# Performance work log

Hardware: AMD Instinct MI355X
Metric: run time of the kernel (lower is better)

The kernel has to match this reference:

```python
import jax, jax.numpy as jnp
import numpy as np

DIM = 1024
HEADS = 16
HEAD_DIM = DIM // HEADS


def setup_inputs() -> dict:
    key = jax.random.key(0)
    ks = jax.random.split(key, 9)
    s = 1.0 / np.sqrt(DIM)
    return {
        "x": jax.random.normal(ks[0], (2, 2048, DIM), dtype=jnp.float32),
        "Wq": jax.random.normal(ks[1], (DIM, DIM), dtype=jnp.float32) * s,
        "bq": jnp.zeros((DIM,), dtype=jnp.float32),
        "Wk": jax.random.normal(ks[2], (DIM, DIM), dtype=jnp.float32) * s,
        "bk": jnp.zeros((DIM,), dtype=jnp.float32),
        "Wv": jax.random.normal(ks[3], (DIM, DIM), dtype=jnp.float32) * s,
        "bv": jnp.zeros((DIM,), dtype=jnp.float32),
        "Wo": jax.random.normal(ks[4], (DIM, DIM), dtype=jnp.float32) * s,
        "bo": jnp.zeros((DIM,), dtype=jnp.float32),
    }


def reference(x, Wq, bq, Wk, bk, Wv, bv, Wo, bo):
    B, S, D = x.shape
    H, Dh = HEADS, HEAD_DIM

    def split_heads(t):  # (B,S,D) -> (B,H,S,Dh)
        return t.reshape(B, S, H, Dh).transpose(0, 2, 1, 3)

    q = split_heads(x @ Wq + bq)
    k = split_heads(x @ Wk + bk)
    v = split_heads(x @ Wv + bv)

    scores = jnp.einsum("bhsd,bhtd->bhst", q, k) / np.sqrt(Dh).astype(x.dtype)
    attn = jax.nn.softmax(scores, axis=-1)
    ctx = jnp.einsum("bhst,bhtd->bhsd", attn, v)
    ctx = ctx.transpose(0, 2, 1, 3).reshape(B, S, D)
    return ctx @ Wo + bo
```

## Files before the change

### kernel.cpp

```cpp
#include <hip/hip_runtime.h>
#include <hip/hip_bf16.h>
#include <cstdint>

typedef __bf16 bf16;
typedef __bf16 bf16x8 __attribute__((ext_vector_type(8)));
typedef float f32x4 __attribute__((ext_vector_type(4)));
typedef float f32x8 __attribute__((ext_vector_type(8)));
typedef float f32x16 __attribute__((ext_vector_type(16)));

#define DIM   1024
#define SEQ   2048
#define BATCH 2
#define HEADS 16
#define HDIM  64

#define QSCALE 0.1803368801111204f

__device__ __forceinline__ void gload_lds16(const void* g, void* l) {
    __builtin_amdgcn_global_load_lds(
        (const __attribute__((address_space(1))) void*)g,
        (__attribute__((address_space(3))) void*)l,
        16, 0, 0);
}

__device__ __forceinline__ uint32_t pkbf(float a, float b) {
    union { bf16 h[2]; uint32_t u; } t;
    t.h[0] = (bf16)a; t.h[1] = (bf16)b;
    return t.u;
}

#define LO8(v)  __builtin_shufflevector(v, v, 0, 1, 2, 3, 4, 5, 6, 7)
#define HI8(v)  __builtin_shufflevector(v, v, 8, 9, 10, 11, 12, 13, 14, 15)
#define LO4(v)  __builtin_shufflevector(v, v, 0, 1, 2, 3)
#define HI4(v)  __builtin_shufflevector(v, v, 4, 5, 6, 7)

__global__ __launch_bounds__(256) void cvt_x_kernel(const float* __restrict__ x,
                                                    bf16* __restrict__ xb) {
    int idx = blockIdx.x * 256 + threadIdx.x;
    const float4* p = (const float4*)(x + (size_t)idx * 8);
    float4 a = p[0], b = p[1];
    bf16x8 o;
    o[0] = (bf16)a.x; o[1] = (bf16)a.y; o[2] = (bf16)a.z; o[3] = (bf16)a.w;
    o[4] = (bf16)b.x; o[5] = (bf16)b.y; o[6] = (bf16)b.z; o[7] = (bf16)b.w;
    *(bf16x8*)(xb + (size_t)idx * 8) = o;
}

__global__ __launch_bounds__(256) void cvt_wt_kernel(const float* __restrict__ Wq,
                                                     const float* __restrict__ Wk,
                                                     const float* __restrict__ Wv,
                                                     const float* __restrict__ Wo,
                                                     bf16* __restrict__ Wt) {
    int z = blockIdx.z;
    const float* W = (z == 0) ? Wq : (z == 1) ? Wk : (z == 2) ? Wv : Wo;
    bf16* out = Wt + (size_t)z * DIM * DIM;
    int w = threadIdx.x >> 6, lane = threadIdx.x & 63;
    int n  = blockIdx.x * 64 + lane;
    int kb = blockIdx.y * 32 + w * 8;
    bf16x8 o;
#pragma unroll
    for (int j = 0; j < 8; ++j)
        o[j] = (bf16)W[(size_t)(kb + j) * DIM + n];
    *(bf16x8*)(out + (size_t)n * DIM + kb) = o;
}

template <int MODE>
__global__ __launch_bounds__(256) void gemm128_kernel(
        const bf16* __restrict__ A,
        const bf16* __restrict__ WtB,
        const float* __restrict__ b0,
        const float* __restrict__ b1,
        const float* __restrict__ b2,
        void* __restrict__ outp) {
    constexpr int K = DIM;
    int z = (MODE == 0) ? blockIdx.z : 0;
    const bf16* Bt = WtB + (size_t)z * DIM * DIM;
    const float* bias = (MODE == 0) ? ((z == 0) ? b0 : (z == 1) ? b1 : b2) : b0;

    int m0 = blockIdx.y * 128, n0 = blockIdx.x * 128;
    int tid = threadIdx.x;
    int w = tid >> 6, lane = tid & 63, l15 = lane & 15, l4 = lane >> 4;
    int wr = (w >> 1) * 64, wc = (w & 1) * 64;

    __shared__ __align__(16) bf16 As[128 * 32];
    __shared__ __align__(16) bf16 Bs[128 * 32];

    f32x4 acc[4][4] = {};

    for (int k0 = 0; k0 < K; k0 += 32) {
#pragma unroll
        for (int r = 0; r < 2; ++r) {
            int c = r * 256 + tid;
            gload_lds16(A  + (size_t)(m0 + (c >> 2)) * K + k0 + (c & 3) * 8, &As[c * 8]);
            gload_lds16(Bt + (size_t)(n0 + (c >> 2)) * K + k0 + (c & 3) * 8, &Bs[c * 8]);
        }
        __syncthreads();
        bf16x8 af[4], bfr[4];
#pragma unroll
        for (int m = 0; m < 4; ++m)
            af[m] = *(const bf16x8*)&As[(wr + m * 16 + l15) * 32 + l4 * 8];
#pragma unroll
        for (int n = 0; n < 4; ++n)
            bfr[n] = *(const bf16x8*)&Bs[(wc + n * 16 + l15) * 32 + l4 * 8];
#pragma unroll
        for (int m = 0; m < 4; ++m)
#pragma unroll
            for (int n = 0; n < 4; ++n)
                acc[m][n] = __builtin_amdgcn_mfma_f32_16x16x32_bf16(
                    af[m], bfr[n], acc[m][n], 0, 0, 0);
        __syncthreads();
    }

    float oscale = (MODE == 0 && z == 0) ? QSCALE : 1.0f;
#pragma unroll
    for (int n = 0; n < 4; ++n) {
        int col = n0 + wc + n * 16 + l15;
        float bv = bias[col];
#pragma unroll
        for (int m = 0; m < 4; ++m) {
            int rowb = m0 + wr + m * 16 + l4 * 4;
            if (MODE == 1) {
                float* out = (float*)outp;
#pragma unroll
                for (int i = 0; i < 4; ++i)
                    out[(size_t)(rowb + i) * DIM + col] = acc[m][n][i] + bv;
            } else if (z < 2) {
                bf16* out = (bf16*)outp + (size_t)z * (BATCH * HEADS * SEQ * HDIM);
                int h = col >> 6, d = col & 63;
#pragma unroll
                for (int i = 0; i < 4; ++i) {
                    int row = rowb + i;
                    int bb = row >> 11, s = row & 2047;
                    out[(((size_t)(bb * HEADS + h)) * SEQ + s) * HDIM + d] =
                        (bf16)((acc[m][n][i] + bv) * oscale);
                }
            } else {
                bf16* out = (bf16*)outp + (size_t)2 * (BATCH * HEADS * SEQ * HDIM);
                int h = col >> 6, d = col & 63;
                int bb = rowb >> 11, s0 = rowb & 2047;
                union { bf16 hh[4]; ushort4 v; } pk;
#pragma unroll
                for (int i = 0; i < 4; ++i) pk.hh[i] = (bf16)(acc[m][n][i] + bv);
                *(ushort4*)&out[(((size_t)(bb * HEADS + h)) * HDIM + d) * SEQ + s0] = pk.v;
            }
        }
    }
}

__global__ __launch_bounds__(256) void attn_kernel(const bf16* __restrict__ Q,
                                                   const bf16* __restrict__ K,
                                                   const bf16* __restrict__ Vt,
                                                   bf16* __restrict__ ctx) {
    int hb = blockIdx.y;
    int bb = hb >> 4, h = hb & 15;
    int q0 = blockIdx.x * 128;
    int tid = threadIdx.x, w = tid >> 6, lane = tid & 63;
    int l31 = lane & 31, hi = lane >> 5;

    const bf16* Qh = Q  + (size_t)hb * SEQ * HDIM;
    const bf16* Kh = K  + (size_t)hb * SEQ * HDIM;
    const bf16* Vh = Vt + (size_t)hb * HDIM * SEQ;

    __shared__ __align__(16) bf16 Ks[2][64 * 64];
    __shared__ __align__(16) bf16 Vs[2][64 * 64];

    int qrow = q0 + w * 32 + l31;
    bf16x8 qf[4];
#pragma unroll
    for (int ks = 0; ks < 4; ++ks)
        qf[ks] = *(const bf16x8*)&Qh[(size_t)qrow * HDIM + ks * 16 + hi * 8];

    f32x16 o0 = {}, o1 = {};
    float l = 0.f;

    const bf16* kbase[2];
    const bf16* vbase[2];
    int ldsoff[2];
#pragma unroll
    for (int r = 0; r < 2; ++r) {
        int c = r * 256 + tid, row = c >> 3, sj = (c & 7) ^ (row & 7);
        kbase[r] = Kh + (size_t)row * HDIM + sj * 8;
        vbase[r] = Vh + (size_t)row * SEQ + sj * 8;
        ldsoff[r] = c * 8;
    }
    auto stage = [&](bf16* ksd, bf16* vsd, int kv0) {
#pragma unroll
        for (int r = 0; r < 2; ++r) {
            gload_lds16(kbase[r] + kv0 * HDIM, ksd + ldsoff[r]);
            gload_lds16(vbase[r] + kv0,        vsd + ldsoff[r]);
        }
    };

    int koffA = l31 * 128;
    int cb[4];
#pragma unroll
    for (int ks = 0; ks < 4; ++ks)
        cb[ks] = ((2 * ks + hi) ^ (l31 & 7)) << 4;

    auto proc = [&](const char* ksb, const char* vsb) {
        f32x16 s0 = {}, s1 = {};
        __builtin_amdgcn_s_setprio(1);
#pragma unroll
        for (int ks = 0; ks < 4; ++ks) {
            bf16x8 k0 = *(const bf16x8*)(ksb + koffA + cb[ks]);
            bf16x8 k1 = *(const bf16x8*)(ksb + koffA + 4096 + cb[ks]);
            s0 = __builtin_amdgcn_mfma_f32_32x32x16_bf16(k0, qf[ks], s0, 0, 0, 0);
            s1 = __builtin_amdgcn_mfma_f32_32x32x16_bf16(k1, qf[ks], s1, 0, 0, 0);
        }
        __builtin_amdgcn_s_setprio(0);

#pragma unroll
        for (int r = 0; r < 16; ++r) {
            s0[r] = __builtin_amdgcn_exp2f(s0[r]);
            s1[r] = __builtin_amdgcn_exp2f(s1[r]);
        }

        f32x16 a16 = s0 + s1;
        f32x8  a8  = LO8(a16) + HI8(a16);
        f32x4  a4  = LO4(a8) + HI4(a8);
        l += (a4[0] + a4[1]) + (a4[2] + a4[3]);

        bf16x8 pa[4];
#pragma unroll
        for (int f = 0; f < 4; ++f) {
            const f32x16& s = (f < 2) ? s0 : s1;
            int rb = (f & 1) * 8;
            uint32_t w0 = pkbf(s[rb + 0], s[rb + 1]), w1 = pkbf(s[rb + 2], s[rb + 3]);
            uint32_t w2 = pkbf(s[rb + 4], s[rb + 5]), w3 = pkbf(s[rb + 6], s[rb + 7]);
            asm("v_permlane32_swap_b32 %0, %1" : "+v"(w0), "+v"(w2));
            asm("v_permlane32_swap_b32 %0, %1" : "+v"(w1), "+v"(w3));
            union { uint32_t u[4]; bf16x8 v; } t2;
            t2.u[0] = w0; t2.u[1] = w1; t2.u[2] = w2; t2.u[3] = w3;
            pa[f] = t2.v;
        }

        __builtin_amdgcn_s_setprio(1);
#pragma unroll
        for (int ks = 0; ks < 4; ++ks) {
            bf16x8 v0 = *(const bf16x8*)(vsb + koffA + cb[ks]);
            bf16x8 v1 = *(const bf16x8*)(vsb + koffA + 4096 + cb[ks]);
            o0 = __builtin_amdgcn_mfma_f32_32x32x16_bf16(v0, pa[ks], o0, 0, 0, 0);
            o1 = __builtin_amdgcn_mfma_f32_32x32x16_bf16(v1, pa[ks], o1, 0, 0, 0);
        }
        __builtin_amdgcn_s_setprio(0);
    };

    constexpr int NT = SEQ / 64;
    stage(Ks[0], Vs[0], 0);
    __syncthreads();

    for (int t = 0; t < NT; t += 2) {
        if (t + 1 < NT) stage(Ks[1], Vs[1], (t + 1) * 64);
        proc((const char*)&Ks[0][0], (const char*)&Vs[0][0]);
        __syncthreads();
        if (t + 2 < NT) stage(Ks[0], Vs[0], (t + 2) * 64);
        proc((const char*)&Ks[1][0], (const char*)&Vs[1][0]);
        __syncthreads();
    }

    l += __shfl_xor(l, 32);
    float inv = 1.0f / l;
    size_t base = ((size_t)bb * SEQ + q0 + w * 32 + l31) * DIM + h * HDIM;
#pragma unroll
    for (int g = 0; g < 4; ++g) {
        int dh0 = 8 * g + 4 * hi;
        union { bf16 hh[4]; ushort4 u; } a, b2;
#pragma unroll
        for (int i = 0; i < 4; ++i) {
            a.hh[i]  = (bf16)(o0[4 * g + i] * inv);
            b2.hh[i] = (bf16)(o1[4 * g + i] * inv);
        }
        *(ushort4*)&ctx[base + dh0]      = a.u;
        *(ushort4*)&ctx[base + 32 + dh0] = b2.u;
    }
}

extern "C" void kernel_launch(void* const* d_in, const int* in_sizes, int n_in,
                              void* d_out, int out_size, void* d_ws, size_t ws_size,
                              hipStream_t stream) {
    const float* x  = (const float*)d_in[0];
    const float* Wq = (const float*)d_in[1];
    const float* bq = (const float*)d_in[2];
    const float* Wk = (const float*)d_in[3];
    const float* bk = (const float*)d_in[4];
    const float* Wv = (const float*)d_in[5];
    const float* bv = (const float*)d_in[6];
    const float* Wo = (const float*)d_in[7];
    const float* bo = (const float*)d_in[8];

    char* ws = (char*)d_ws;
    bf16* xb  = (bf16*)(ws);
    bf16* Wt  = (bf16*)(ws + (8u  << 20));
    bf16* Qb  = (bf16*)(ws + (16u << 20));
    bf16* Kb  = (bf16*)(ws + (24u << 20));
    bf16* Vb  = (bf16*)(ws + (32u << 20));
    bf16* ctx = (bf16*)(ws + (40u << 20));

    cvt_x_kernel<<<2048, 256, 0, stream>>>(x, xb);
    cvt_wt_kernel<<<dim3(16, 32, 4), 256, 0, stream>>>(Wq, Wk, Wv, Wo, Wt);
    gemm128_kernel<0><<<dim3(8, 32, 3), 256, 0, stream>>>(xb, Wt, bq, bk, bv, (void*)Qb);
    attn_kernel<<<dim3(16, 32), 256, 0, stream>>>(Qb, Kb, Vb, ctx);
    gemm128_kernel<1><<<dim3(8, 32, 1), 256, 0, stream>>>(
        ctx, Wt + (size_t)3 * DIM * DIM, bo, bo, bo, (void*)d_out);
}
```

Baseline: 125.2 us.

## Load K/V fragments directly from global into registers, dropping LDS staging

```diff
diff --git a/kernel.cpp b/kernel.cpp
--- a/kernel.cpp
+++ b/kernel.cpp
@@ -146,10 +146,12 @@
     }
 }
 
-__global__ __launch_bounds__(256) void attn_kernel(const bf16* __restrict__ Q,
-                                                   const bf16* __restrict__ K,
-                                                   const bf16* __restrict__ Vt,
-                                                   bf16* __restrict__ ctx) {
+struct KVFrags { bf16x8 k0[4], k1[4], v0[4], v1[4]; };
+
+__global__ __launch_bounds__(256, 2) void attn_kernel(const bf16* __restrict__ Q,
+                                                      const bf16* __restrict__ K,
+                                                      const bf16* __restrict__ Vt,
+                                                      bf16* __restrict__ ctx) {
     int hb = blockIdx.y;
     int bb = hb >> 4, h = hb & 15;
     int q0 = blockIdx.x * 128;
@@ -157,11 +159,8 @@
     int l31 = lane & 31, hi = lane >> 5;
 
     const bf16* Qh = Q  + (size_t)hb * SEQ * HDIM;
-    const bf16* Kh = K  + (size_t)hb * SEQ * HDIM;
-    const bf16* Vh = Vt + (size_t)hb * HDIM * SEQ;
-
-    __shared__ __align__(16) bf16 Ks[2][64 * 64];
-    __shared__ __align__(16) bf16 Vs[2][64 * 64];
+    const bf16* kbase = K  + (size_t)hb * SEQ * HDIM + (size_t)l31 * HDIM + hi * 8;
+    const bf16* vbase = Vt + (size_t)hb * HDIM * SEQ + (size_t)l31 * SEQ  + hi * 8;
 
     int qrow = q0 + w * 32 + l31;
     bf16x8 qf[4];
@@ -172,39 +171,25 @@
     f32x16 o0 = {}, o1 = {};
     float l = 0.f;
 
-    const bf16* kbase[2];
-    const bf16* vbase[2];
-    int ldsoff[2];
-#pragma unroll
-    for (int r = 0; r < 2; ++r) {
-        int c = r * 256 + tid, row = c >> 3, sj = (c & 7) ^ (row & 7);
-        kbase[r] = Kh + (size_t)row * HDIM + sj * 8;
-        vbase[r] = Vh + (size_t)row * SEQ + sj * 8;
-        ldsoff[r] = c * 8;
-    }
-    auto stage = [&](bf16* ksd, bf16* vsd, int kv0) {
-#pragma unroll
-        for (int r = 0; r < 2; ++r) {
-            gload_lds16(kbase[r] + kv0 * HDIM, ksd + ldsoff[r]);
-            gload_lds16(vbase[r] + kv0,        vsd + ldsoff[r]);
+    auto load = [&](KVFrags& f, int kv0) {
+        const bf16* kp = kbase + (size_t)kv0 * HDIM;
+        const bf16* vp = vbase + kv0;
+#pragma unroll
+        for (int ks = 0; ks < 4; ++ks) {
+            f.k0[ks] = *(const bf16x8*)(kp + ks * 16);
+            f.k1[ks] = *(const bf16x8*)(kp + 32 * HDIM + ks * 16);
+            f.v0[ks] = *(const bf16x8*)(vp + ks * 16);
+            f.v1[ks] = *(const bf16x8*)(vp + 32 * SEQ + ks * 16);
         }
     };
 
-    int koffA = l31 * 128;
-    int cb[4];
-#pragma unroll
-    for (int ks = 0; ks < 4; ++ks)
-        cb[ks] = ((2 * ks + hi) ^ (l31 & 7)) << 4;
-
-    auto proc = [&](const char* ksb, const char* vsb) {
+    auto compute = [&](const KVFrags& f) {
         f32x16 s0 = {}, s1 = {};
         __builtin_amdgcn_s_setprio(1);
 #pragma unroll
         for (int ks = 0; ks < 4; ++ks) {
-            bf16x8 k0 = *(const bf16x8*)(ksb + koffA + cb[ks]);
-            bf16x8 k1 = *(const bf16x8*)(ksb + koffA + 4096 + cb[ks]);
-            s0 = __builtin_amdgcn_mfma_f32_32x32x16_bf16(k0, qf[ks], s0, 0, 0, 0);
-            s1 = __builtin_amdgcn_mfma_f32_32x32x16_bf16(k1, qf[ks], s1, 0, 0, 0);
+            s0 = __builtin_amdgcn_mfma_f32_32x32x16_bf16(f.k0[ks], qf[ks], s0, 0, 0, 0);
+            s1 = __builtin_amdgcn_mfma_f32_32x32x16_bf16(f.k1[ks], qf[ks], s1, 0, 0, 0);
         }
         __builtin_amdgcn_s_setprio(0);
 
@@ -221,40 +206,36 @@
 
         bf16x8 pa[4];
 #pragma unroll
-        for (int f = 0; f < 4; ++f) {
-            const f32x16& s = (f < 2) ? s0 : s1;
-            int rb = (f & 1) * 8;
+        for (int f2 = 0; f2 < 4; ++f2) {
+            const f32x16& s = (f2 < 2) ? s0 : s1;
+            int rb = (f2 & 1) * 8;
             uint32_t w0 = pkbf(s[rb + 0], s[rb + 1]), w1 = pkbf(s[rb + 2], s[rb + 3]);
             uint32_t w2 = pkbf(s[rb + 4], s[rb + 5]), w3 = pkbf(s[rb + 6], s[rb + 7]);
             asm("v_permlane32_swap_b32 %0, %1" : "+v"(w0), "+v"(w2));
             asm("v_permlane32_swap_b32 %0, %1" : "+v"(w1), "+v"(w3));
             union { uint32_t u[4]; bf16x8 v; } t2;
             t2.u[0] = w0; t2.u[1] = w1; t2.u[2] = w2; t2.u[3] = w3;
-            pa[f] = t2.v;
+            pa[f2] = t2.v;
         }
 
         __builtin_amdgcn_s_setprio(1);
 #pragma unroll
         for (int ks = 0; ks < 4; ++ks) {
-            bf16x8 v0 = *(const bf16x8*)(vsb + koffA + cb[ks]);
-            bf16x8 v1 = *(const bf16x8*)(vsb + koffA + 4096 + cb[ks]);
-            o0 = __builtin_amdgcn_mfma_f32_32x32x16_bf16(v0, pa[ks], o0, 0, 0, 0);
-            o1 = __builtin_amdgcn_mfma_f32_32x32x16_bf16(v1, pa[ks], o1, 0, 0, 0);
+            o0 = __builtin_amdgcn_mfma_f32_32x32x16_bf16(f.v0[ks], pa[ks], o0, 0, 0, 0);
+            o1 = __builtin_amdgcn_mfma_f32_32x32x16_bf16(f.v1[ks], pa[ks], o1, 0, 0, 0);
         }
         __builtin_amdgcn_s_setprio(0);
     };
 
     constexpr int NT = SEQ / 64;
-    stage(Ks[0], Vs[0], 0);
-    __syncthreads();
+    KVFrags fa, fb;
+    load(fa, 0);
 
     for (int t = 0; t < NT; t += 2) {
-        if (t + 1 < NT) stage(Ks[1], Vs[1], (t + 1) * 64);
-        proc((const char*)&Ks[0][0], (const char*)&Vs[0][0]);
-        __syncthreads();
-        if (t + 2 < NT) stage(Ks[0], Vs[0], (t + 2) * 64);
-        proc((const char*)&Ks[1][0], (const char*)&Vs[1][0]);
-        __syncthreads();
+        if (t + 1 < NT) load(fb, (t + 1) * 64);
+        compute(fa);
+        if (t + 2 < NT) load(fa, (t + 2) * 64);
+        compute(fb);
     }
 
     l += __shfl_xor(l, 32);
```

Result: slower. 195.2 us (+55.8%).

## Split attention KV range across two blocks and merge partial outputs

Applied to the files above, without the earlier changes.

```diff
diff --git a/kernel.cpp b/kernel.cpp
--- a/kernel.cpp
+++ b/kernel.cpp
@@ -149,10 +149,14 @@
 __global__ __launch_bounds__(256) void attn_kernel(const bf16* __restrict__ Q,
                                                    const bf16* __restrict__ K,
                                                    const bf16* __restrict__ Vt,
-                                                   bf16* __restrict__ ctx) {
+                                                   bf16* __restrict__ opA,
+                                                   bf16* __restrict__ opB,
+                                                   float* __restrict__ lbuf) {
     int hb = blockIdx.y;
     int bb = hb >> 4, h = hb & 15;
     int q0 = blockIdx.x * 128;
+    int si = blockIdx.z;
+    int kvb = si * (SEQ / 2);
     int tid = threadIdx.x, w = tid >> 6, lane = tid & 63;
     int l31 = lane & 31, hi = lane >> 5;
 
@@ -185,8 +189,8 @@
     auto stage = [&](bf16* ksd, bf16* vsd, int kv0) {
 #pragma unroll
         for (int r = 0; r < 2; ++r) {
-            gload_lds16(kbase[r] + kv0 * HDIM, ksd + ldsoff[r]);
-            gload_lds16(vbase[r] + kv0,        vsd + ldsoff[r]);
+            gload_lds16(kbase[r] + (size_t)kv0 * HDIM, ksd + ldsoff[r]);
+            gload_lds16(vbase[r] + kv0,                vsd + ldsoff[r]);
         }
     };
 
@@ -221,16 +225,16 @@
 
         bf16x8 pa[4];
 #pragma unroll
-        for (int f = 0; f < 4; ++f) {
-            const f32x16& s = (f < 2) ? s0 : s1;
-            int rb = (f & 1) * 8;
+        for (int f2 = 0; f2 < 4; ++f2) {
+            const f32x16& s = (f2 < 2) ? s0 : s1;
+            int rb = (f2 & 1) * 8;
             uint32_t w0 = pkbf(s[rb + 0], s[rb + 1]), w1 = pkbf(s[rb + 2], s[rb + 3]);
             uint32_t w2 = pkbf(s[rb + 4], s[rb + 5]), w3 = pkbf(s[rb + 6], s[rb + 7]);
             asm("v_permlane32_swap_b32 %0, %1" : "+v"(w0), "+v"(w2));
             asm("v_permlane32_swap_b32 %0, %1" : "+v"(w1), "+v"(w3));
             union { uint32_t u[4]; bf16x8 v; } t2;
             t2.u[0] = w0; t2.u[1] = w1; t2.u[2] = w2; t2.u[3] = w3;
-            pa[f] = t2.v;
+            pa[f2] = t2.v;
         }
 
         __builtin_amdgcn_s_setprio(1);
@@ -244,34 +248,59 @@
         __builtin_amdgcn_s_setprio(0);
     };
 
-    constexpr int NT = SEQ / 64;
-    stage(Ks[0], Vs[0], 0);
+    constexpr int NT = (SEQ / 2) / 64;
+    stage(Ks[0], Vs[0], kvb);
     __syncthreads();
 
     for (int t = 0; t < NT; t += 2) {
-        if (t + 1 < NT) stage(Ks[1], Vs[1], (t + 1) * 64);
+        if (t + 1 < NT) stage(Ks[1], Vs[1], kvb + (t + 1) * 64);
         proc((const char*)&Ks[0][0], (const char*)&Vs[0][0]);
         __syncthreads();
-        if (t + 2 < NT) stage(Ks[0], Vs[0], (t + 2) * 64);
+        if (t + 2 < NT) stage(Ks[0], Vs[0], kvb + (t + 2) * 64);
         proc((const char*)&Ks[1][0], (const char*)&Vs[1][0]);
         __syncthreads();
     }
 
     l += __shfl_xor(l, 32);
-    float inv = 1.0f / l;
-    size_t base = ((size_t)bb * SEQ + q0 + w * 32 + l31) * DIM + h * HDIM;
+    bf16* op = si ? opB : opA;
+    if (hi == 0)
+        lbuf[((size_t)si * BATCH * HEADS + hb) * SEQ + qrow] = l;
+    size_t base = ((size_t)bb * SEQ + qrow) * DIM + h * HDIM;
 #pragma unroll
     for (int g = 0; g < 4; ++g) {
         int dh0 = 8 * g + 4 * hi;
         union { bf16 hh[4]; ushort4 u; } a, b2;
 #pragma unroll
         for (int i = 0; i < 4; ++i) {
-            a.hh[i]  = (bf16)(o0[4 * g + i] * inv);
-            b2.hh[i] = (bf16)(o1[4 * g + i] * inv);
-        }
-        *(ushort4*)&ctx[base + dh0]      = a.u;
-        *(ushort4*)&ctx[base + 32 + dh0] = b2.u;
-    }
+            a.hh[i]  = (bf16)o0[4 * g + i];
+            b2.hh[i] = (bf16)o1[4 * g + i];
+        }
+        *(ushort4*)&op[base + dh0]      = a.u;
+        *(ushort4*)&op[base + 32 + dh0] = b2.u;
+    }
+}
+
+__global__ __launch_bounds__(256) void merge_kernel(const bf16* __restrict__ opA,
+                                                    const bf16* __restrict__ opB,
+                                                    const float* __restrict__ lbuf,
+                                                    bf16* __restrict__ ctx) {
+    int idx = blockIdx.x * 256 + threadIdx.x;
+    size_t e8 = (size_t)idx * 8;
+    int row = (int)(e8 >> 10);
+    int d   = (int)(e8 & 1023);
+    int h = d >> 6;
+    int bb = row >> 11, s = row & 2047;
+    int hb = bb * HEADS + h;
+    float la = lbuf[(size_t)hb * SEQ + s];
+    float lb = lbuf[((size_t)BATCH * HEADS + hb) * SEQ + s];
+    float inv = 1.0f / (la + lb);
+    bf16x8 a = *(const bf16x8*)&opA[e8];
+    bf16x8 b = *(const bf16x8*)&opB[e8];
+    bf16x8 o;
+#pragma unroll
+    for (int i = 0; i < 8; ++i)
+        o[i] = (bf16)(((float)a[i] + (float)b[i]) * inv);
+    *(bf16x8*)&ctx[e8] = o;
 }
 
 extern "C" void kernel_launch(void* const* d_in, const int* in_sizes, int n_in,
@@ -295,10 +324,15 @@
     bf16* Vb  = (bf16*)(ws + (32u << 20));
     bf16* ctx = (bf16*)(ws + (40u << 20));
 
+    bf16*  opA  = ctx;
+    bf16*  opB  = xb;
+    float* lbuf = (float*)Wt;
+
     cvt_x_kernel<<<2048, 256, 0, stream>>>(x, xb);
     cvt_wt_kernel<<<dim3(16, 32, 4), 256, 0, stream>>>(Wq, Wk, Wv, Wo, Wt);
     gemm128_kernel<0><<<dim3(8, 32, 3), 256, 0, stream>>>(xb, Wt, bq, bk, bv, (void*)Qb);
-    attn_kernel<<<dim3(16, 32), 256, 0, stream>>>(Qb, Kb, Vb, ctx);
+    attn_kernel<<<dim3(16, 32, 2), 256, 0, stream>>>(Qb, Kb, Vb, opA, opB, lbuf);
+    merge_kernel<<<2048, 256, 0, stream>>>(opA, opB, lbuf, ctx);
     gemm128_kernel<1><<<dim3(8, 32, 1), 256, 0, stream>>>(
         ctx, Wt + (size_t)3 * DIM * DIM, bo, bo, bo, (void*)d_out);
 }
```

After: 131.8 us. 5.2% more time.

## Fuse x fp32-to-bf16 conversion into QKV GEMM and double attention KV tile

Applied to the files above, without the earlier changes.

```diff
diff --git a/kernel.cpp b/kernel.cpp
--- a/kernel.cpp
+++ b/kernel.cpp
@@ -33,17 +33,6 @@
 #define HI8(v)  __builtin_shufflevector(v, v, 8, 9, 10, 11, 12, 13, 14, 15)
 #define LO4(v)  __builtin_shufflevector(v, v, 0, 1, 2, 3)
 #define HI4(v)  __builtin_shufflevector(v, v, 4, 5, 6, 7)
-
-__global__ __launch_bounds__(256) void cvt_x_kernel(const float* __restrict__ x,
-                                                    bf16* __restrict__ xb) {
-    int idx = blockIdx.x * 256 + threadIdx.x;
-    const float4* p = (const float4*)(x + (size_t)idx * 8);
-    float4 a = p[0], b = p[1];
-    bf16x8 o;
-    o[0] = (bf16)a.x; o[1] = (bf16)a.y; o[2] = (bf16)a.z; o[3] = (bf16)a.w;
-    o[4] = (bf16)b.x; o[5] = (bf16)b.y; o[6] = (bf16)b.z; o[7] = (bf16)b.w;
-    *(bf16x8*)(xb + (size_t)idx * 8) = o;
-}
 
 __global__ __launch_bounds__(256) void cvt_wt_kernel(const float* __restrict__ Wq,
                                                      const float* __restrict__ Wk,
@@ -65,7 +54,7 @@
 
 template <int MODE>
 __global__ __launch_bounds__(256) void gemm128_kernel(
-        const bf16* __restrict__ A,
+        const void* __restrict__ Ap,
         const bf16* __restrict__ WtB,
         const float* __restrict__ b0,
         const float* __restrict__ b1,
@@ -84,14 +73,35 @@
     __shared__ __align__(16) bf16 As[128 * 32];
     __shared__ __align__(16) bf16 Bs[128 * 32];
 
+    int arow = tid >> 1, acol = (tid & 1) * 16;
+    const float* asrc = (MODE == 0)
+        ? (const float*)Ap + (size_t)(m0 + arow) * K + acol : nullptr;
+
     f32x4 acc[4][4] = {};
 
     for (int k0 = 0; k0 < K; k0 += 32) {
 #pragma unroll
         for (int r = 0; r < 2; ++r) {
             int c = r * 256 + tid;
-            gload_lds16(A  + (size_t)(m0 + (c >> 2)) * K + k0 + (c & 3) * 8, &As[c * 8]);
             gload_lds16(Bt + (size_t)(n0 + (c >> 2)) * K + k0 + (c & 3) * 8, &Bs[c * 8]);
+        }
+        if constexpr (MODE == 0) {
+            const float4* s4 = (const float4*)(asrc + k0);
+            float4 f0 = s4[0], f1 = s4[1], f2 = s4[2], f3 = s4[3];
+            bf16x8 e0, e1;
+            e0[0] = (bf16)f0.x; e0[1] = (bf16)f0.y; e0[2] = (bf16)f0.z; e0[3] = (bf16)f0.w;
+            e0[4] = (bf16)f1.x; e0[5] = (bf16)f1.y; e0[6] = (bf16)f1.z; e0[7] = (bf16)f1.w;
+            e1[0] = (bf16)f2.x; e1[1] = (bf16)f2.y; e1[2] = (bf16)f2.z; e1[3] = (bf16)f2.w;
+            e1[4] = (bf16)f3.x; e1[5] = (bf16)f3.y; e1[6] = (bf16)f3.z; e1[7] = (bf16)f3.w;
+            *(bf16x8*)&As[arow * 32 + acol]     = e0;
+            *(bf16x8*)&As[arow * 32 + acol + 8] = e1;
+        } else {
+            const bf16* A = (const bf16*)Ap;
+#pragma unroll
+            for (int r = 0; r < 2; ++r) {
+                int c = r * 256 + tid;
+                gload_lds16(A + (size_t)(m0 + (c >> 2)) * K + k0 + (c & 3) * 8, &As[c * 8]);
+            }
         }
         __syncthreads();
         bf16x8 af[4], bfr[4];
@@ -160,8 +170,8 @@
     const bf16* Kh = K  + (size_t)hb * SEQ * HDIM;
     const bf16* Vh = Vt + (size_t)hb * HDIM * SEQ;
 
-    __shared__ __align__(16) bf16 Ks[2][64 * 64];
-    __shared__ __align__(16) bf16 Vs[2][64 * 64];
+    __shared__ __align__(16) bf16 Ks[2][8192];
+    __shared__ __align__(16) bf16 Vs[2][8192];
 
     int qrow = q0 + w * 32 + l31;
     bf16x8 qf[4];
@@ -177,16 +187,20 @@
     int ldsoff[2];
 #pragma unroll
     for (int r = 0; r < 2; ++r) {
-        int c = r * 256 + tid, row = c >> 3, sj = (c & 7) ^ (row & 7);
-        kbase[r] = Kh + (size_t)row * HDIM + sj * 8;
-        vbase[r] = Vh + (size_t)row * SEQ + sj * 8;
+        int c = r * 256 + tid;
+        int krow = c >> 3, kj = (c & 7) ^ (krow & 7);
+        kbase[r] = Kh + (size_t)krow * HDIM + kj * 8;
+        int dh = (c >> 3) & 63, vj = (c & 7) ^ (dh & 7);
+        vbase[r] = Vh + (size_t)dh * SEQ + vj * 8;
         ldsoff[r] = c * 8;
     }
     auto stage = [&](bf16* ksd, bf16* vsd, int kv0) {
 #pragma unroll
         for (int r = 0; r < 2; ++r) {
-            gload_lds16(kbase[r] + kv0 * HDIM, ksd + ldsoff[r]);
-            gload_lds16(vbase[r] + kv0,        vsd + ldsoff[r]);
+            gload_lds16(kbase[r] + (size_t)kv0 * HDIM,        ksd + ldsoff[r]);
+            gload_lds16(kbase[r] + (size_t)(kv0 + 64) * HDIM, ksd + ldsoff[r] + 4096);
+            gload_lds16(vbase[r] + kv0,                       vsd + ldsoff[r]);
+            gload_lds16(vbase[r] + kv0 + 64,                  vsd + ldsoff[r] + 4096);
         }
     };
 
@@ -196,13 +210,13 @@
     for (int ks = 0; ks < 4; ++ks)
         cb[ks] = ((2 * ks + hi) ^ (l31 & 7)) << 4;
 
-    auto proc = [&](const char* ksb, const char* vsb) {
+    auto sub64 = [&](const char* kp, const char* vp) {
         f32x16 s0 = {}, s1 = {};
         __builtin_amdgcn_s_setprio(1);
 #pragma unroll
         for (int ks = 0; ks < 4; ++ks) {
-            bf16x8 k0 = *(const bf16x8*)(ksb + koffA + cb[ks]);
-            bf16x8 k1 = *(const bf16x8*)(ksb + koffA + 4096 + cb[ks]);
+            bf16x8 k0 = *(const bf16x8*)(kp + koffA + cb[ks]);
+            bf16x8 k1 = *(const bf16x8*)(kp + koffA + 4096 + cb[ks]);
             s0 = __builtin_amdgcn_mfma_f32_32x32x16_bf16(k0, qf[ks], s0, 0, 0, 0);
             s1 = __builtin_amdgcn_mfma_f32_32x32x16_bf16(k1, qf[ks], s1, 0, 0, 0);
         }
@@ -221,45 +235,50 @@
 
         bf16x8 pa[4];
 #pragma unroll
-        for (int f = 0; f < 4; ++f) {
-            const f32x16& s = (f < 2) ? s0 : s1;
-            int rb = (f & 1) * 8;
+        for (int f2 = 0; f2 < 4; ++f2) {
+            const f32x16& s = (f2 < 2) ? s0 : s1;
+            int rb = (f2 & 1) * 8;
             uint32_t w0 = pkbf(s[rb + 0], s[rb + 1]), w1 = pkbf(s[rb + 2], s[rb + 3]);
             uint32_t w2 = pkbf(s[rb + 4], s[rb + 5]), w3 = pkbf(s[rb + 6], s[rb + 7]);
             asm("v_permlane32_swap_b32 %0, %1" : "+v"(w0), "+v"(w2));
             asm("v_permlane32_swap_b32 %0, %1" : "+v"(w1), "+v"(w3));
             union { uint32_t u[4]; bf16x8 v; } t2;
             t2.u[0] = w0; t2.u[1] = w1; t2.u[2] = w2; t2.u[3] = w3;
-            pa[f] = t2.v;
+            pa[f2] = t2.v;
         }
 
         __builtin_amdgcn_s_setprio(1);
 #pragma unroll
         for (int ks = 0; ks < 4; ++ks) {
-            bf16x8 v0 = *(const bf16x8*)(vsb + koffA + cb[ks]);
-            bf16x8 v1 = *(const bf16x8*)(vsb + koffA + 4096 + cb[ks]);
+            bf16x8 v0 = *(const bf16x8*)(vp + koffA + cb[ks]);
+            bf16x8 v1 = *(const bf16x8*)(vp + koffA + 4096 + cb[ks]);
             o0 = __builtin_amdgcn_mfma_f32_32x32x16_bf16(v0, pa[ks], o0, 0, 0, 0);
             o1 = __builtin_amdgcn_mfma_f32_32x32x16_bf16(v1, pa[ks], o1, 0, 0, 0);
         }
         __builtin_amdgcn_s_setprio(0);
     };
 
-    constexpr int NT = SEQ / 64;
+    auto proc = [&](const char* ksb, const char* vsb) {
+        sub64(ksb, vsb);
+        sub64(ksb + 8192, vsb + 8192);
+    };
+
+    constexpr int NT = SEQ / 128;
     stage(Ks[0], Vs[0], 0);
     __syncthreads();
 
     for (int t = 0; t < NT; t += 2) {
-        if (t + 1 < NT) stage(Ks[1], Vs[1], (t + 1) * 64);
+        if (t + 1 < NT) stage(Ks[1], Vs[1], (t + 1) * 128);
         proc((const char*)&Ks[0][0], (const char*)&Vs[0][0]);
         __syncthreads();
-        if (t + 2 < NT) stage(Ks[0], Vs[0], (t + 2) * 64);
+        if (t + 2 < NT) stage(Ks[0], Vs[0], (t + 2) * 128);
         proc((const char*)&Ks[1][0], (const char*)&Vs[1][0]);
         __syncthreads();
     }
 
     l += __shfl_xor(l, 32);
     float inv = 1.0f / l;
-    size_t base = ((size_t)bb * SEQ + q0 + w * 32 + l31) * DIM + h * HDIM;
+    size_t base = ((size_t)bb * SEQ + qrow) * DIM + h * HDIM;
 #pragma unroll
     for (int g = 0; g < 4; ++g) {
         int dh0 = 8 * g + 4 * hi;
@@ -288,16 +307,14 @@
     const float* bo = (const float*)d_in[8];
 
     char* ws = (char*)d_ws;
-    bf16* xb  = (bf16*)(ws);
     bf16* Wt  = (bf16*)(ws + (8u  << 20));
     bf16* Qb  = (bf16*)(ws + (16u << 20));
     bf16* Kb  = (bf16*)(ws + (24u << 20));
     bf16* Vb  = (bf16*)(ws + (32u << 20));
     bf16* ctx = (bf16*)(ws + (40u << 20));
 
-    cvt_x_kernel<<<2048, 256, 0, stream>>>(x, xb);
     cvt_wt_kernel<<<dim3(16, 32, 4), 256, 0, stream>>>(Wq, Wk, Wv, Wo, Wt);
-    gemm128_kernel<0><<<dim3(8, 32, 3), 256, 0, stream>>>(xb, Wt, bq, bk, bv, (void*)Qb);
+    gemm128_kernel<0><<<dim3(8, 32, 3), 256, 0, stream>>>(x, Wt, bq, bk, bv, (void*)Qb);
     attn_kernel<<<dim3(16, 32), 256, 0, stream>>>(Qb, Kb, Vb, ctx);
     gemm128_kernel<1><<<dim3(8, 32, 1), 256, 0, stream>>>(
         ctx, Wt + (size_t)3 * DIM * DIM, bo, bo, bo, (void*)d_out);
```

Result: no change. 123.8 us (-1.1%).
